# Kernel optimization log

Hardware: AMD Instinct MI355X
Metric: run time of the kernel (lower is better)

Reference implementation:

```python
import jax, jax.numpy as jnp
import numpy as np
from jax import lax

B, T, D, L = 64, 512, 1024, 32


def setup_inputs() -> dict:
    key = jax.random.key(0)
    ks = jax.random.split(key, 6)
    embeddings = jax.random.normal(ks[0], (B, T, D), dtype=jnp.float32)
    W = jax.random.normal(ks[1], (L, D), dtype=jnp.float32) * (1.0 / np.sqrt(D))
    b = jnp.zeros((L,), dtype=jnp.float32)
    start_trans = jax.random.normal(ks[2], (L,), dtype=jnp.float32) * 0.1
    end_trans = jax.random.normal(ks[3], (L,), dtype=jnp.float32) * 0.1
    trans = jax.random.normal(ks[4], (L, L), dtype=jnp.float32) * 0.1
    labels = jax.random.randint(ks[5], (B, T), 0, L, dtype=jnp.int32)
    mask = jnp.ones((B, T), dtype=bool)  # torchcrf requires mask[:, 0] == True
    return {"embeddings": embeddings, "W": W, "b": b,
            "start_trans": start_trans, "end_trans": end_trans,
            "trans": trans, "labels": labels, "mask": mask}


def _crf_nll(emissions, labels, mask, start_trans, end_trans, trans):
    # emissions: [B, T, L]; torchcrf works time-first internally.
    em = jnp.transpose(emissions, (1, 0, 2))          # [T, B, L]
    tg = labels.T                                      # [T, B]
    mk_b = mask.T                                      # [T, B] bool
    mk_f = mk_b.astype(emissions.dtype)
    bidx = jnp.arange(em.shape[1])

    # ---- numerator: score of the gold tag path ----
    score0 = start_trans[tg[0]] + em[0, bidx, tg[0]]   # [B]

    def num_step(carry, inp):
        prev_tag, score = carry
        e_t, tag_t, m_b, m_f = inp
        step = trans[prev_tag, tag_t] + e_t[bidx, tag_t]
        score = score + step * m_f
        prev_tag = jnp.where(m_b, tag_t, prev_tag)
        return (prev_tag, score), None

    (last_tag, num), _ = lax.scan(num_step, (tg[0], score0),
                                  (em[1:], tg[1:], mk_b[1:], mk_f[1:]))
    num = num + end_trans[last_tag]

    # ---- denominator: forward algorithm (log partition) ----
    alpha0 = start_trans[None, :] + em[0]              # [B, L]

    def den_step(alpha, inp):
        e_t, m_b = inp
        # alpha[b, i] + trans[i, j] + e_t[b, j] -> logsumexp over i
        nxt = jax.nn.logsumexp(alpha[:, :, None] + trans[None, :, :]
                               + e_t[:, None, :], axis=1)
        alpha = jnp.where(m_b[:, None], nxt, alpha)
        return alpha, None

    alpha, _ = lax.scan(den_step, alpha0, (em[1:], mk_b[1:]))
    den = jax.nn.logsumexp(alpha + end_trans[None, :], axis=1)  # [B]

    llh = num - den                                    # log-likelihood per seq
    return -jnp.mean(llh)                              # reduction='mean', negated


def reference(embeddings, W, b, start_trans, end_trans, trans, labels, mask):
    # dropout is identity at eval time
    emissions = jnp.einsum('btd,ld->btl', embeddings, W) + b  # [B, T, L]
    return _crf_nll(emissions, labels, mask, start_trans, end_trans, trans)
```

## Files before the change

### kernel.cpp

```cpp
#include <hip/hip_runtime.h>
#include <hip/hip_bf16.h>

#define NB 64
#define NT 512
#define ND 1024
#define NL 32
#define SEG 16
#define NSEG 32

typedef __attribute__((ext_vector_type(8)))  short bf16x8;
typedef __attribute__((ext_vector_type(4)))  float f32x4;
typedef __attribute__((ext_vector_type(16))) float f32x16;

__device__ __forceinline__ unsigned short bfh(float x) {
    __hip_bfloat16 h = __float2bfloat16(x);
    return *(unsigned short*)&h;
}
__device__ __forceinline__ float frombf(unsigned short u) {
    return __uint_as_float(((unsigned)u) << 16);
}
__device__ __forceinline__ bf16x8 pack8(float4 x, float4 y) {
    bf16x8 r;
    unsigned short* p = (unsigned short*)&r;
    p[0] = bfh(x.x); p[1] = bfh(x.y); p[2] = bfh(x.z); p[3] = bfh(x.w);
    p[4] = bfh(y.x); p[5] = bfh(y.y); p[6] = bfh(y.z); p[7] = bfh(y.w);
    return r;
}
__device__ __forceinline__ bf16x8 mk8(unsigned a, unsigned b, unsigned c, unsigned d) {
    union { unsigned u[4]; bf16x8 v; } t;
    t.u[0] = a; t.u[1] = b; t.u[2] = c; t.u[3] = d;
    return t.v;
}
__device__ __forceinline__ void pl32swap(unsigned& x, unsigned& y) {
    asm volatile("v_permlane32_swap_b32 %0, %1" : "+v"(x), "+v"(y));
}

__global__ __launch_bounds__(256) void wb_kernel(
    const float* __restrict__ W, unsigned short* __restrict__ Wb,
    int* __restrict__ cnt)
{
    if (blockIdx.x == 0 && threadIdx.x == 0) *cnt = 0;
    int i = blockIdx.x * 256 + threadIdx.x;
    float4 v = ((const float4*)W)[i];
    ushort4 o;
    o.x = bfh(v.x); o.y = bfh(v.y); o.z = bfh(v.z); o.w = bfh(v.w);
    ((ushort4*)Wb)[i] = o;
}

struct Grp {
    float4 a[4][2];
    bf16x8 b[4][2];
};

__device__ __forceinline__ void load_grp(
    Grp& G, const float* __restrict__ ap,
    const unsigned short* __restrict__ bp0,
    const unsigned short* __restrict__ bp1, int k0)
{
#pragma unroll
    for (int s = 0; s < 4; s++) {
        G.a[s][0] = *(const float4*)(ap + k0 + s * 32);
        G.a[s][1] = *(const float4*)(ap + k0 + s * 32 + 4);
        G.b[s][0] = *(const bf16x8*)(bp0 + k0 + s * 32);
        G.b[s][1] = *(const bf16x8*)(bp1 + k0 + s * 32);
    }
}

__global__ __launch_bounds__(256) void emseg_kernel(
    const float* __restrict__ emb,
    const unsigned short* __restrict__ Wb,
    const float* __restrict__ bias,
    const float* __restrict__ start_trans,
    const float* __restrict__ trans,
    const int*   __restrict__ labels,
    float* __restrict__ Pm,
    int*   __restrict__ exps,
    float* __restrict__ numpart)
{
    __shared__ float em_s[4][SEG][36];

    const int tid  = threadIdx.x;
    const int wv   = tid >> 6;
    const int lane = tid & 63;
    const int m    = lane & 15;
    const int quad = lane >> 4;
    const int w    = blockIdx.x * 4 + wv;
    const int b    = w >> 5;
    const int s    = w & 31;
    const int row  = w * 16 + m;
    const int t0   = s * SEG;

    const float*          ap  = emb + (size_t)row * ND + quad * 8;
    const unsigned short* bp0 = Wb + (size_t)m * ND + quad * 8;
    const unsigned short* bp1 = Wb + (size_t)(16 + m) * ND + quad * 8;

    f32x4 acc0 = {0.f, 0.f, 0.f, 0.f};
    f32x4 acc1 = {0.f, 0.f, 0.f, 0.f};

    Grp g0, g1;
    load_grp(g0, ap, bp0, bp1, 0);
    load_grp(g1, ap, bp0, bp1, 128);

#pragma unroll
    for (int g = 0; g < 8; g++) {
        Grp& cur = (g & 1) ? g1 : g0;
#pragma unroll
        for (int st = 0; st < 4; st++) {
            bf16x8 af = pack8(cur.a[st][0], cur.a[st][1]);
            acc0 = __builtin_amdgcn_mfma_f32_16x16x32_bf16(af, cur.b[st][0], acc0, 0, 0, 0);
            acc1 = __builtin_amdgcn_mfma_f32_16x16x32_bf16(af, cur.b[st][1], acc1, 0, 0, 0);
        }
        if (g < 6) load_grp(cur, ap, bp0, bp1, (g + 2) * 128);
    }

    const float bl0 = bias[m];
    const float bl1 = bias[16 + m];
#pragma unroll
    for (int r = 0; r < 4; r++) {
        int lt = quad * 4 + r;
        em_s[wv][lt][m]      = __expf(acc0[r] + bl0);
        em_s[wv][lt][16 + m] = __expf(acc1[r] + bl1);
    }
    asm volatile("s_waitcnt lgkmcnt(0)" ::: "memory");

    {
        const int* lab = labels + b * NT;
        float npart = 0.f;
        if (lane < SEG) {
            int t = t0 + lane;
            if (t >= 1) {
                int pt = lab[t - 1], ct = lab[t];
                npart = trans[pt * NL + ct] + __logf(em_s[wv][lane][ct]);
            } else {
                int c0 = lab[0];
                npart = start_trans[c0] + __logf(em_s[wv][0][c0]);
            }
        }
#pragma unroll
        for (int mk = 32; mk >= 1; mk >>= 1) npart += __shfl_xor(npart, mk, 64);
        if (lane == 0) numpart[b * NSEG + s] = npart;
    }

    const int col = lane & 31;
    const int h   = lane >> 5;
    const int ls  = (s == 0) ? 1 : 0;

    bf16x8 Eh1, Eh2, El1, El2;
#pragma unroll
    for (int j = 0; j < 8; j++) {
        float v1 = __expf(trans[(8 * h + j) * NL + col]);
        float v2 = __expf(trans[(16 + 8 * h + j) * NL + col]);
        unsigned short h1 = bfh(v1), h2 = bfh(v2);
        ((unsigned short*)&Eh1)[j] = h1;
        ((unsigned short*)&Eh2)[j] = h2;
        ((unsigned short*)&El1)[j] = bfh(v1 - frombf(h1));
        ((unsigned short*)&El2)[j] = bfh(v2 - frombf(h2));
    }

    bf16x8 Qh1, Qh2, Ql1, Ql2;
    {
        float sA = 1.f;
        if (s == 0) sA = __expf(start_trans[col]) * em_s[wv][0][col];
#pragma unroll
        for (int j = 0; j < 8; j++) {
            int k1 = 8 * h + j, k2 = 16 + 8 * h + j;
            float v1 = sA * __expf(trans[col * NL + k1]) * em_s[wv][ls][k1];
            float v2 = sA * __expf(trans[col * NL + k2]) * em_s[wv][ls][k2];
            unsigned short h1 = bfh(v1), h2 = bfh(v2);
            ((unsigned short*)&Qh1)[j] = h1;
            ((unsigned short*)&Qh2)[j] = h2;
            ((unsigned short*)&Ql1)[j] = bfh(v1 - frombf(h1));
            ((unsigned short*)&Ql2)[j] = bfh(v2 - frombf(h2));
        }
    }

    int eseg = 0;
    for (int lt = ls + 1; lt < SEG; lt++) {
        f32x16 accA, accB;
#pragma unroll
        for (int i = 0; i < 16; i++) { accA[i] = 0.f; accB[i] = 0.f; }
        accA = __builtin_amdgcn_mfma_f32_32x32x16_bf16(Eh1, Qh1, accA, 0, 0, 0);
        accB = __builtin_amdgcn_mfma_f32_32x32x16_bf16(Eh2, Qh2, accB, 0, 0, 0);
        accA = __builtin_amdgcn_mfma_f32_32x32x16_bf16(Eh1, Ql1, accA, 0, 0, 0);
        accB = __builtin_amdgcn_mfma_f32_32x32x16_bf16(Eh2, Ql2, accB, 0, 0, 0);
        accA = __builtin_amdgcn_mfma_f32_32x32x16_bf16(El1, Qh1, accA, 0, 0, 0);
        accB = __builtin_amdgcn_mfma_f32_32x32x16_bf16(El2, Qh2, accB, 0, 0, 0);

        const float* emrow = &em_s[wv][lt][4 * h];
        float4 e0 = *(const float4*)(emrow);
        float4 e1 = *(const float4*)(emrow + 8);
        float4 e2 = *(const float4*)(emrow + 16);
        float4 e3 = *(const float4*)(emrow + 24);
        float v[16];
        v[0]  = (accA[0]  + accB[0])  * e0.x;
        v[1]  = (accA[1]  + accB[1])  * e0.y;
        v[2]  = (accA[2]  + accB[2])  * e0.z;
        v[3]  = (accA[3]  + accB[3])  * e0.w;
        v[4]  = (accA[4]  + accB[4])  * e1.x;
        v[5]  = (accA[5]  + accB[5])  * e1.y;
        v[6]  = (accA[6]  + accB[6])  * e1.z;
        v[7]  = (accA[7]  + accB[7])  * e1.w;
        v[8]  = (accA[8]  + accB[8])  * e2.x;
        v[9]  = (accA[9]  + accB[9])  * e2.y;
        v[10] = (accA[10] + accB[10]) * e2.z;
        v[11] = (accA[11] + accB[11]) * e2.w;
        v[12] = (accA[12] + accB[12]) * e3.x;
        v[13] = (accA[13] + accB[13]) * e3.y;
        v[14] = (accA[14] + accB[14]) * e3.z;
        v[15] = (accA[15] + accB[15]) * e3.w;

        int bits = __builtin_amdgcn_readlane(__float_as_int(v[0]), 0);
        int e = (bits >> 23) & 255;
        eseg += e - 127;
        float scale = __uint_as_float((unsigned)(254 - e) << 23);

        if (lt < SEG - 1) {
            unsigned hw[8], lw[8];
#pragma unroll
            for (int g = 0; g < 8; g++) {
                float va = v[2 * g] * scale;
                float vb = v[2 * g + 1] * scale;
                unsigned short ha = bfh(va), hb = bfh(vb);
                hw[g] = ((unsigned)hb << 16) | ha;
                unsigned short la = bfh(va - frombf(ha));
                unsigned short lb = bfh(vb - frombf(hb));
                lw[g] = ((unsigned)lb << 16) | la;
            }
            pl32swap(hw[0], hw[2]); pl32swap(hw[1], hw[3]);
            pl32swap(hw[4], hw[6]); pl32swap(hw[5], hw[7]);
            pl32swap(lw[0], lw[2]); pl32swap(lw[1], lw[3]);
            pl32swap(lw[4], lw[6]); pl32swap(lw[5], lw[7]);
            Qh1 = mk8(hw[0], hw[1], hw[2], hw[3]);
            Qh2 = mk8(hw[4], hw[5], hw[6], hw[7]);
            Ql1 = mk8(lw[0], lw[1], lw[2], lw[3]);
            Ql2 = mk8(lw[4], lw[5], lw[6], lw[7]);
        } else {
            float* dst = Pm + ((size_t)(b * NSEG + s) << 10);
#pragma unroll
            for (int r = 0; r < 16; r++) {
                int rowi = (r & 3) + 8 * (r >> 2) + 4 * h;
                dst[rowi * 32 + col] = v[r] * scale;
            }
        }
    }
    if (lane == 0) exps[b * NSEG + s] = eseg;
}

__global__ __launch_bounds__(64) void comb_kernel(
    const float* __restrict__ end_trans,
    const float* __restrict__ Pm,
    const int*   __restrict__ exps,
    const float* __restrict__ numpart,
    const int*   __restrict__ labels,
    float* __restrict__ den_out,
    float* __restrict__ num_out,
    int*   __restrict__ cnt,
    float* __restrict__ out)
{
    const int b    = blockIdx.x;
    const int lane = threadIdx.x;
    const int col  = lane & 31;

    int sexp = 0;
    float sv[32];
#pragma unroll
    for (int i = 0; i < 32; i++) sv[i] = 1.0f;

    const float* Pb = Pm + ((size_t)b * NSEG << 10);
    float Pc[32];
#pragma unroll
    for (int g = 0; g < 8; g++) {
        float4 q = *(const float4*)(Pb + col * 32 + 4 * g);
        Pc[4 * g] = q.x; Pc[4 * g + 1] = q.y;
        Pc[4 * g + 2] = q.z; Pc[4 * g + 3] = q.w;
    }

    float a = 0.f;
    for (int s = 0; s < NSEG; s++) {
        float nb[32];
        if (s + 1 < NSEG) {
            const float* q = Pb + ((size_t)(s + 1) << 10) + col * 32;
#pragma unroll
            for (int g = 0; g < 8; g++) {
                float4 t = *(const float4*)(q + 4 * g);
                nb[4 * g] = t.x; nb[4 * g + 1] = t.y;
                nb[4 * g + 2] = t.z; nb[4 * g + 3] = t.w;
            }
        } else {
#pragma unroll
            for (int i = 0; i < 32; i++) nb[i] = 0.f;
        }

        float p0 = sv[0] * Pc[0], p1 = sv[1] * Pc[1];
        float p2 = sv[2] * Pc[2], p3 = sv[3] * Pc[3];
        float p4 = sv[4] * Pc[4], p5 = sv[5] * Pc[5];
        float p6 = sv[6] * Pc[6], p7 = sv[7] * Pc[7];
#pragma unroll
        for (int i = 8; i < 32; i += 8) {
            p0 = fmaf(sv[i + 0], Pc[i + 0], p0);
            p1 = fmaf(sv[i + 1], Pc[i + 1], p1);
            p2 = fmaf(sv[i + 2], Pc[i + 2], p2);
            p3 = fmaf(sv[i + 3], Pc[i + 3], p3);
            p4 = fmaf(sv[i + 4], Pc[i + 4], p4);
            p5 = fmaf(sv[i + 5], Pc[i + 5], p5);
            p6 = fmaf(sv[i + 6], Pc[i + 6], p6);
            p7 = fmaf(sv[i + 7], Pc[i + 7], p7);
        }
        a = (((p0 + p1) + (p2 + p3)) + ((p4 + p5) + (p6 + p7)));

        int bits = __builtin_amdgcn_readlane(__float_as_int(a), 0);
        int e = (bits >> 23) & 255;
        sexp += e - 127;
        a *= __uint_as_float((unsigned)(254 - e) << 23);

#pragma unroll
        for (int i = 0; i < 32; i++)
            sv[i] = __int_as_float(__builtin_amdgcn_readlane(__float_as_int(a), i));
#pragma unroll
        for (int i = 0; i < 32; i++) Pc[i] = nb[i];
    }

    float sege = (lane < NSEG) ? (float)exps[b * NSEG + lane] : 0.f;
#pragma unroll
    for (int mk = 32; mk >= 1; mk >>= 1) sege += __shfl_xor(sege, mk, 64);

    float x = a * __expf(end_trans[col]);
#pragma unroll
    for (int mk = 16; mk >= 1; mk >>= 1) x += __shfl_xor(x, mk, 32);

    float nsum = (lane < NSEG) ? numpart[b * NSEG + lane] : 0.f;
#pragma unroll
    for (int mk = 32; mk >= 1; mk >>= 1) nsum += __shfl_xor(nsum, mk, 64);

    int ticket = 0;
    if (lane == 0) {
        int lT = labels[b * NT + NT - 1];
        num_out[b] = nsum + end_trans[lT];
        den_out[b] = __logf(x)
                   + 0.69314718055994531f * ((float)sexp + sege);
        __threadfence();
        ticket = atomicAdd(cnt, 1);
    }
    ticket = __shfl(ticket, 0, 64);
    if (ticket == NB - 1) {
        __threadfence();
        float v = den_out[lane] - num_out[lane];
#pragma unroll
        for (int mk = 32; mk >= 1; mk >>= 1) v += __shfl_xor(v, mk, 64);
        if (lane == 0) out[0] = v * (1.0f / 64.0f);
    }
}

extern "C" void kernel_launch(void* const* d_in, const int* in_sizes, int n_in,
                              void* d_out, int out_size, void* d_ws, size_t ws_size,
                              hipStream_t stream)
{
    const float* emb    = (const float*)d_in[0];
    const float* W      = (const float*)d_in[1];
    const float* bias   = (const float*)d_in[2];
    const float* st     = (const float*)d_in[3];
    const float* en     = (const float*)d_in[4];
    const float* tr     = (const float*)d_in[5];
    const int*   labels = (const int*)d_in[6];

    char* p = (char*)d_ws;
    float* Pm  = (float*)p;                  p += (size_t)NB * NSEG * 1024 * 4;
    int*   exps = (int*)p;                   p += NB * NSEG * 4;
    float* nump = (float*)p;                 p += NB * NSEG * 4;
    float* den  = (float*)p;                 p += NB * 4;
    float* num  = (float*)p;                 p += NB * 4;
    int*   cnt  = (int*)p;                   p += 256;
    unsigned short* Wb = (unsigned short*)p;
    float* out = (float*)d_out;

    wb_kernel   <<<(NL * ND) / 1024, 256, 0, stream>>>(W, Wb, cnt);
    emseg_kernel<<<(NB * NT) / 64, 256, 0, stream>>>(emb, Wb, bias, st, tr,
                                                     labels, Pm, exps, nump);
    comb_kernel <<<NB, 64, 0, stream>>>(en, Pm, exps, nump, labels, den, num,
                                        cnt, out);
}
```

Baseline: 243.4 us.

## Fuse segment-combine into emission kernel via per-batch last-block ticket

Removes the separate comb_kernel launch. Each emseg block bumps a per-batch atomic counter once its segments are written. The last of the 8 blocks for a batch element then runs the sequential segment-product combine in its first wavefront. This overlaps the combine with remaining emission work and drops one launch boundary, at the cost of extra fences, atomics and register pressure in the fused kernel.

New measurement: 290.0 us. +19.2%, slower.

```diff
diff --git a/kernel.cpp b/kernel.cpp
--- a/kernel.cpp
+++ b/kernel.cpp
@@ -39,7 +39,7 @@
     const float* __restrict__ W, unsigned short* __restrict__ Wb,
     int* __restrict__ cnt)
 {
-    if (blockIdx.x == 0 && threadIdx.x == 0) *cnt = 0;
+    if (blockIdx.x == 0 && threadIdx.x < 65) cnt[threadIdx.x] = 0;
     int i = blockIdx.x * 256 + threadIdx.x;
     float4 v = ((const float4*)W)[i];
     ushort4 o;
@@ -71,13 +71,19 @@
     const unsigned short* __restrict__ Wb,
     const float* __restrict__ bias,
     const float* __restrict__ start_trans,
+    const float* __restrict__ end_trans,
     const float* __restrict__ trans,
     const int*   __restrict__ labels,
     float* __restrict__ Pm,
     int*   __restrict__ exps,
-    float* __restrict__ numpart)
+    float* __restrict__ numpart,
+    float* __restrict__ den_out,
+    float* __restrict__ num_out,
+    int*   __restrict__ cnt,
+    float* __restrict__ out)
 {
     __shared__ float em_s[4][SEG][36];
+    __shared__ int   tick_s;
 
     const int tid  = threadIdx.x;
     const int wv   = tid >> 6;
@@ -244,110 +250,103 @@
         }
     }
     if (lane == 0) exps[b * NSEG + s] = eseg;
-}
-
-__global__ __launch_bounds__(64) void comb_kernel(
-    const float* __restrict__ end_trans,
-    const float* __restrict__ Pm,
-    const int*   __restrict__ exps,
-    const float* __restrict__ numpart,
-    const int*   __restrict__ labels,
-    float* __restrict__ den_out,
-    float* __restrict__ num_out,
-    int*   __restrict__ cnt,
-    float* __restrict__ out)
-{
-    const int b    = blockIdx.x;
-    const int lane = threadIdx.x;
-    const int col  = lane & 31;
-
-    int sexp = 0;
-    float sv[32];
-#pragma unroll
-    for (int i = 0; i < 32; i++) sv[i] = 1.0f;
-
-    const float* Pb = Pm + ((size_t)b * NSEG << 10);
-    float Pc[32];
-#pragma unroll
-    for (int g = 0; g < 8; g++) {
-        float4 q = *(const float4*)(Pb + col * 32 + 4 * g);
-        Pc[4 * g] = q.x; Pc[4 * g + 1] = q.y;
-        Pc[4 * g + 2] = q.z; Pc[4 * g + 3] = q.w;
-    }
-
-    float a = 0.f;
-    for (int s = 0; s < NSEG; s++) {
-        float nb[32];
-        if (s + 1 < NSEG) {
-            const float* q = Pb + ((size_t)(s + 1) << 10) + col * 32;
-#pragma unroll
-            for (int g = 0; g < 8; g++) {
-                float4 t = *(const float4*)(q + 4 * g);
-                nb[4 * g] = t.x; nb[4 * g + 1] = t.y;
-                nb[4 * g + 2] = t.z; nb[4 * g + 3] = t.w;
-            }
-        } else {
-#pragma unroll
-            for (int i = 0; i < 32; i++) nb[i] = 0.f;
-        }
-
-        float p0 = sv[0] * Pc[0], p1 = sv[1] * Pc[1];
-        float p2 = sv[2] * Pc[2], p3 = sv[3] * Pc[3];
-        float p4 = sv[4] * Pc[4], p5 = sv[5] * Pc[5];
-        float p6 = sv[6] * Pc[6], p7 = sv[7] * Pc[7];
-#pragma unroll
-        for (int i = 8; i < 32; i += 8) {
-            p0 = fmaf(sv[i + 0], Pc[i + 0], p0);
-            p1 = fmaf(sv[i + 1], Pc[i + 1], p1);
-            p2 = fmaf(sv[i + 2], Pc[i + 2], p2);
-            p3 = fmaf(sv[i + 3], Pc[i + 3], p3);
-            p4 = fmaf(sv[i + 4], Pc[i + 4], p4);
-            p5 = fmaf(sv[i + 5], Pc[i + 5], p5);
-            p6 = fmaf(sv[i + 6], Pc[i + 6], p6);
-            p7 = fmaf(sv[i + 7], Pc[i + 7], p7);
-        }
-        a = (((p0 + p1) + (p2 + p3)) + ((p4 + p5) + (p6 + p7)));
-
-        int bits = __builtin_amdgcn_readlane(__float_as_int(a), 0);
-        int e = (bits >> 23) & 255;
-        sexp += e - 127;
-        a *= __uint_as_float((unsigned)(254 - e) << 23);
-
-#pragma unroll
-        for (int i = 0; i < 32; i++)
-            sv[i] = __int_as_float(__builtin_amdgcn_readlane(__float_as_int(a), i));
-#pragma unroll
-        for (int i = 0; i < 32; i++) Pc[i] = nb[i];
-    }
-
-    float sege = (lane < NSEG) ? (float)exps[b * NSEG + lane] : 0.f;
-#pragma unroll
-    for (int mk = 32; mk >= 1; mk >>= 1) sege += __shfl_xor(sege, mk, 64);
-
-    float x = a * __expf(end_trans[col]);
-#pragma unroll
-    for (int mk = 16; mk >= 1; mk >>= 1) x += __shfl_xor(x, mk, 32);
-
-    float nsum = (lane < NSEG) ? numpart[b * NSEG + lane] : 0.f;
-#pragma unroll
-    for (int mk = 32; mk >= 1; mk >>= 1) nsum += __shfl_xor(nsum, mk, 64);
-
-    int ticket = 0;
-    if (lane == 0) {
-        int lT = labels[b * NT + NT - 1];
-        num_out[b] = nsum + end_trans[lT];
-        den_out[b] = __logf(x)
-                   + 0.69314718055994531f * ((float)sexp + sege);
-        __threadfence();
-        ticket = atomicAdd(cnt, 1);
-    }
-    ticket = __shfl(ticket, 0, 64);
-    if (ticket == NB - 1) {
-        __threadfence();
-        float v = den_out[lane] - num_out[lane];
-#pragma unroll
-        for (int mk = 32; mk >= 1; mk >>= 1) v += __shfl_xor(v, mk, 64);
-        if (lane == 0) out[0] = v * (1.0f / 64.0f);
+
+    __threadfence();
+    __syncthreads();
+    if (tid == 0) tick_s = atomicAdd(&cnt[1 + b], 1);
+    __syncthreads();
+    if (tick_s != 7 || wv != 0) return;
+
+    __threadfence();
+    {
+        int sexp = 0;
+        float sv[32];
+#pragma unroll
+        for (int i = 0; i < 32; i++) sv[i] = 1.0f;
+
+        const float* Pb = Pm + ((size_t)b * NSEG << 10);
+        float Pc[32];
+#pragma unroll
+        for (int g = 0; g < 8; g++) {
+            float4 q = *(const float4*)(Pb + col * 32 + 4 * g);
+            Pc[4 * g] = q.x; Pc[4 * g + 1] = q.y;
+            Pc[4 * g + 2] = q.z; Pc[4 * g + 3] = q.w;
+        }
+
+        float a = 0.f;
+        for (int ss = 0; ss < NSEG; ss++) {
+            float nb[32];
+            if (ss + 1 < NSEG) {
+                const float* q = Pb + ((size_t)(ss + 1) << 10) + col * 32;
+#pragma unroll
+                for (int g = 0; g < 8; g++) {
+                    float4 t = *(const float4*)(q + 4 * g);
+                    nb[4 * g] = t.x; nb[4 * g + 1] = t.y;
+                    nb[4 * g + 2] = t.z; nb[4 * g + 3] = t.w;
+                }
+            } else {
+#pragma unroll
+                for (int i = 0; i < 32; i++) nb[i] = 0.f;
+            }
+
+            float p0 = sv[0] * Pc[0], p1 = sv[1] * Pc[1];
+            float p2 = sv[2] * Pc[2], p3 = sv[3] * Pc[3];
+            float p4 = sv[4] * Pc[4], p5 = sv[5] * Pc[5];
+            float p6 = sv[6] * Pc[6], p7 = sv[7] * Pc[7];
+#pragma unroll
+            for (int i = 8; i < 32; i += 8) {
+                p0 = fmaf(sv[i + 0], Pc[i + 0], p0);
+                p1 = fmaf(sv[i + 1], Pc[i + 1], p1);
+                p2 = fmaf(sv[i + 2], Pc[i + 2], p2);
+                p3 = fmaf(sv[i + 3], Pc[i + 3], p3);
+                p4 = fmaf(sv[i + 4], Pc[i + 4], p4);
+                p5 = fmaf(sv[i + 5], Pc[i + 5], p5);
+                p6 = fmaf(sv[i + 6], Pc[i + 6], p6);
+                p7 = fmaf(sv[i + 7], Pc[i + 7], p7);
+            }
+            a = (((p0 + p1) + (p2 + p3)) + ((p4 + p5) + (p6 + p7)));
+
+            int bits = __builtin_amdgcn_readlane(__float_as_int(a), 0);
+            int e = (bits >> 23) & 255;
+            sexp += e - 127;
+            a *= __uint_as_float((unsigned)(254 - e) << 23);
+
+#pragma unroll
+            for (int i = 0; i < 32; i++)
+                sv[i] = __int_as_float(__builtin_amdgcn_readlane(__float_as_int(a), i));
+#pragma unroll
+            for (int i = 0; i < 32; i++) Pc[i] = nb[i];
+        }
+
+        float sege = (lane < NSEG) ? (float)exps[b * NSEG + lane] : 0.f;
+#pragma unroll
+        for (int mk = 32; mk >= 1; mk >>= 1) sege += __shfl_xor(sege, mk, 64);
+
+        float x = a * __expf(end_trans[col]);
+#pragma unroll
+        for (int mk = 16; mk >= 1; mk >>= 1) x += __shfl_xor(x, mk, 32);
+
+        float nsum = (lane < NSEG) ? numpart[b * NSEG + lane] : 0.f;
+#pragma unroll
+        for (int mk = 32; mk >= 1; mk >>= 1) nsum += __shfl_xor(nsum, mk, 64);
+
+        int g = 0;
+        if (lane == 0) {
+            int lT = labels[b * NT + NT - 1];
+            num_out[b] = nsum + end_trans[lT];
+            den_out[b] = __logf(x)
+                       + 0.69314718055994531f * ((float)sexp + sege);
+            __threadfence();
+            g = atomicAdd(&cnt[0], 1);
+        }
+        g = __shfl(g, 0, 64);
+        if (g == NB - 1) {
+            __threadfence();
+            float fv = den_out[lane] - num_out[lane];
+#pragma unroll
+            for (int mk = 32; mk >= 1; mk >>= 1) fv += __shfl_xor(fv, mk, 64);
+            if (lane == 0) out[0] = fv * (1.0f / 64.0f);
+        }
     }
 }
 
@@ -369,13 +368,12 @@
     float* nump = (float*)p;                 p += NB * NSEG * 4;
     float* den  = (float*)p;                 p += NB * 4;
     float* num  = (float*)p;                 p += NB * 4;
-    int*   cnt  = (int*)p;                   p += 256;
+    int*   cnt  = (int*)p;                   p += 512;
     unsigned short* Wb = (unsigned short*)p;
     float* out = (float*)d_out;
 
     wb_kernel   <<<(NL * ND) / 1024, 256, 0, stream>>>(W, Wb, cnt);
-    emseg_kernel<<<(NB * NT) / 64, 256, 0, stream>>>(emb, Wb, bias, st, tr,
-                                                     labels, Pm, exps, nump);
-    comb_kernel <<<NB, 64, 0, stream>>>(en, Pm, exps, nump, labels, den, num,
-                                        cnt, out);
-}
+    emseg_kernel<<<(NB * NT) / 64, 256, 0, stream>>>(emb, Wb, bias, st, en, tr,
+                                                     labels, Pm, exps, nump,
+                                                     den, num, cnt, out);
+}
```
